# Kernel optimization log

Measured on AMD Instinct MI355X. Metric: run time of the kernel, lower is better.

Reference implementation:

```python
import jax, jax.numpy as jnp
import numpy as np

N_USERS = 200000
N_ITEMS = 100000
EMBED_DIM = 64
N_LAYERS = 3
N_INTER = 1000000


def setup_inputs() -> dict:
    key = jax.random.key(0)
    k1, k2, k3, k4 = jax.random.split(key, 4)
    user_ids = jax.random.randint(k1, (N_INTER,), 0, N_USERS, dtype=jnp.int64 if jax.config.jax_enable_x64 else jnp.int32)
    item_ids = jax.random.randint(k2, (N_INTER,), 0, N_ITEMS, dtype=jnp.int64 if jax.config.jax_enable_x64 else jnp.int32)
    user_emb = jax.random.normal(k3, (N_USERS, EMBED_DIM), dtype=jnp.float32) * 0.1
    item_emb = jax.random.normal(k4, (N_ITEMS, EMBED_DIM), dtype=jnp.float32) * 0.1
    return {"user_emb": user_emb, "item_emb": item_emb, "user_ids": user_ids, "item_ids": item_ids}


def reference(user_emb, item_emb, user_ids, item_ids):
    n_users = user_emb.shape[0]
    n_items = item_emb.shape[0]
    n_nodes = n_users + n_items

    # Symmetric bipartite adjacency as directed edge list (both directions).
    src = jnp.concatenate([user_ids, item_ids + n_users])   # [2E]
    dst = jnp.concatenate([item_ids + n_users, user_ids])   # [2E]

    # Symmetric normalization D^{-1/2} A D^{-1/2} (duplicate edges sum, matching scipy CSR).
    deg = jax.ops.segment_sum(jnp.ones_like(src, dtype=jnp.float32), src, num_segments=n_nodes)
    d_inv_sqrt = jnp.where(deg > 0, jax.lax.rsqrt(jnp.maximum(deg, 1.0)), 0.0)
    w = d_inv_sqrt[src] * d_inv_sqrt[dst]                    # [2E] edge weights

    emb = jnp.concatenate([user_emb, item_emb], axis=0)      # [n_nodes, d]
    acc = emb
    for _ in range(N_LAYERS):
        # SpMM: out[dst] += w * emb[src]
        emb = jax.ops.segment_sum(w[:, None] * emb[src], dst, num_segments=n_nodes)
        acc = acc + emb
    final = acc / (N_LAYERS + 1)                             # mean over stacked layers
    return final[:n_users], final[n_users:]
```

## Files before the change

### kernel.cpp

```cpp
#include <hip/hip_runtime.h>

#define N_USERS 200000
#define N_ITEMS 100000
#define N_NODES 300000
#define DIM 64
#define N_INTER 1000000

#define BSHIFT 10
#define BNODES (1 << BSHIFT)
#define NBUCKET ((N_NODES + BNODES - 1) >> BSHIFT)
#define TILE 4096
#define NBLK_P ((N_INTER + TILE - 1) / TILE)

#define NPW 8
#define NWAVE ((N_NODES + NPW - 1) / NPW)
#define GATHER_THREADS (NWAVE * 64)

typedef unsigned short bf16_t;
typedef unsigned int u32;

static __device__ __forceinline__ bf16_t f2bf(float f) {
    union { float f; u32 u; } v; v.f = f;
    u32 r = v.u + 0x7FFFu + ((v.u >> 16) & 1u);
    return (bf16_t)(r >> 16);
}
static __device__ __forceinline__ float bf2f(bf16_t h) {
    union { u32 u; float f; } v; v.u = ((u32)h) << 16;
    return v.f;
}

__global__ void hist_kernel(const int* __restrict__ uid, const int* __restrict__ iid,
                            u32* __restrict__ bucket_count) {
    __shared__ u32 h[NBUCKET];
    int t = threadIdx.x;
    for (int i = t; i < NBUCKET; i += 256) h[i] = 0;
    __syncthreads();
    int base = blockIdx.x * TILE;
    int end = base + TILE; if (end > N_INTER) end = N_INTER;
    for (int k = base + t; k < end; k += 256) {
        int u = uid[k];
        int it = N_USERS + iid[k];
        atomicAdd(&h[it >> BSHIFT], 1u);
        atomicAdd(&h[u >> BSHIFT], 1u);
    }
    __syncthreads();
    for (int i = t; i < NBUCKET; i += 256)
        if (h[i]) atomicAdd(&bucket_count[i], h[i]);
}

__global__ void scan_kernel(const u32* __restrict__ bucket_count, u32* __restrict__ bstart,
                            u32* __restrict__ bucket_cursor, u32* __restrict__ rowptr) {
    __shared__ u32 buf[2][512];
    int t = threadIdx.x;
    u32 v0 = (t < NBUCKET) ? bucket_count[t] : 0u;
    buf[0][t] = v0;
    __syncthreads();
    int s = 0;
    for (int off = 1; off < 512; off <<= 1) {
        u32 v = buf[s][t];
        if (t >= off) v += buf[s][t - off];
        buf[1 - s][t] = v;
        __syncthreads();
        s = 1 - s;
    }
    if (t < NBUCKET) {
        u32 excl = buf[s][t] - v0;
        bstart[t] = excl;
        bucket_cursor[t] = excl;
    }
    if (t == 0) {
        bstart[NBUCKET] = 2 * N_INTER;
        rowptr[N_NODES] = 2 * N_INTER;
    }
}

__global__ void place_kernel(const int* __restrict__ uid, const int* __restrict__ iid,
                             u32* __restrict__ bucket_cursor, u32* __restrict__ bdata) {
    __shared__ u32 h[NBUCKET];
    __shared__ u32 basesh[NBUCKET];
    int t = threadIdx.x;
    for (int i = t; i < NBUCKET; i += 256) h[i] = 0;
    __syncthreads();
    int base = blockIdx.x * TILE;
    int end = base + TILE; if (end > N_INTER) end = N_INTER;
    for (int k = base + t; k < end; k += 256) {
        int u = uid[k];
        int it = N_USERS + iid[k];
        atomicAdd(&h[it >> BSHIFT], 1u);
        atomicAdd(&h[u >> BSHIFT], 1u);
    }
    __syncthreads();
    for (int i = t; i < NBUCKET; i += 256) {
        u32 c = h[i];
        basesh[i] = c ? atomicAdd(&bucket_cursor[i], c) : 0u;
        h[i] = 0;
    }
    __syncthreads();
    for (int k = base + t; k < end; k += 256) {
        int u = uid[k];
        int it = N_USERS + iid[k];
        {
            int b = it >> BSHIFT;
            u32 pos = basesh[b] + atomicAdd(&h[b], 1u);
            bdata[pos] = (((u32)(it & (BNODES - 1))) << 19) | (u32)u;
        }
        {
            int b = u >> BSHIFT;
            u32 pos = basesh[b] + atomicAdd(&h[b], 1u);
            bdata[pos] = (((u32)(u & (BNODES - 1))) << 19) | (u32)it;
        }
    }
}

__global__ void csr_kernel(const u32* __restrict__ bstart, const u32* __restrict__ bdata,
                           u32* __restrict__ rowptr, float* __restrict__ dinv,
                           int* __restrict__ col) {
    __shared__ u32 cnt[BNODES];
    __shared__ u32 sb[2][BNODES];
    __shared__ u32 cur[BNODES];
    int b = blockIdx.x;
    int t = threadIdx.x;
    int nbase = b << BSHIFT;
    u32 bs = bstart[b], be = bstart[b + 1];
    u32 m = be - bs;

    #pragma unroll
    for (int j = 0; j < 4; ++j) cnt[t + j * 256] = 0;
    __syncthreads();
    for (u32 e = t; e < m; e += 256) {
        u32 v = bdata[bs + e];
        atomicAdd(&cnt[v >> 19], 1u);
    }
    __syncthreads();
    #pragma unroll
    for (int j = 0; j < 4; ++j) sb[0][t + j * 256] = cnt[t + j * 256];
    __syncthreads();
    int s = 0;
    for (int off = 1; off < BNODES; off <<= 1) {
        #pragma unroll
        for (int j = 0; j < 4; ++j) {
            int idx = t + j * 256;
            u32 v = sb[s][idx];
            if (idx >= off) v += sb[s][idx - off];
            sb[1 - s][idx] = v;
        }
        __syncthreads();
        s = 1 - s;
    }
    #pragma unroll
    for (int j = 0; j < 4; ++j) {
        int idx = t + j * 256;
        int node = nbase + idx;
        u32 c = cnt[idx];
        u32 excl = sb[s][idx] - c;
        cur[idx] = excl;
        if (node < N_NODES) {
            rowptr[node] = bs + excl;
            dinv[node] = (c > 0) ? rsqrtf((float)c) : 0.0f;
        }
    }
    __syncthreads();
    for (u32 e = t; e < m; e += 256) {
        u32 v = bdata[bs + e];
        u32 ln = v >> 19;
        u32 pos = atomicAdd(&cur[ln], 1u);
        col[bs + pos] = (int)(v & 0x7FFFFu);
    }
}

__global__ void ecol_kernel(const int* __restrict__ col, const float* __restrict__ dinv,
                            int2* __restrict__ ecol) {
    int e = blockIdx.x * blockDim.x + threadIdx.x;
    if (e < 2 * N_INTER) {
        int s = col[e];
        ecol[e] = make_int2(s, __float_as_int(dinv[s]));
    }
}

__global__ void init_kernel(const float4* __restrict__ ue, const float4* __restrict__ ie,
                            ushort4* __restrict__ cur) {
    int idx = blockIdx.x * blockDim.x + threadIdx.x;
    if (idx < N_NODES * 16) {
        float4 v = (idx < N_USERS * 16) ? ue[idx] : ie[idx - N_USERS * 16];
        ushort4 h;
        h.x = f2bf(v.x); h.y = f2bf(v.y); h.z = f2bf(v.z); h.w = f2bf(v.w);
        cur[idx] = h;
    }
}

__global__ void gather_kernel(const u32* __restrict__ rowptr, const int2* __restrict__ ecol,
                              const float* __restrict__ dinv,
                              const bf16_t* __restrict__ cur, bf16_t* __restrict__ nxt) {
    int wid = (blockIdx.x * blockDim.x + threadIdx.x) >> 6;
    int lane = threadIdx.x & 63;
    int n0 = __builtin_amdgcn_readfirstlane(wid * NPW);
    if (n0 >= N_NODES) return;
    u32 rp[NPW + 1];
    #pragma unroll
    for (int i = 0; i <= NPW; ++i) rp[i] = rowptr[n0 + i];
    u32 eend = rp[NPW];
    u32 cbase = rp[0];
    int2 e = make_int2(0, 0);
    {
        u32 cc = eend - cbase; if (cc > 64) cc = 64;
        if ((u32)lane < cc) e = ecol[cbase + lane];
    }
    u32 pos = rp[0];
    #pragma unroll
    for (int r = 0; r < NPW; ++r) {
        u32 re = rp[r + 1];
        float acc = 0.0f;
        while (pos < re) {
            u32 cend = cbase + 64;
            u32 lim = re < cend ? re : cend;
            for (u32 p = pos; p < lim; p += 8) {
                #pragma unroll
                for (int k = 0; k < 8; ++k) {
                    u32 ei = p + (u32)k;
                    int lidx = (ei < lim) ? (int)(ei - cbase) : 0;
                    lidx = __builtin_amdgcn_readfirstlane(lidx);
                    int s = __builtin_amdgcn_readlane(e.x, lidx);
                    int wb = (ei < lim) ? __builtin_amdgcn_readlane(e.y, lidx) : 0;
                    acc += __int_as_float(wb) * bf2f(cur[((u32)s << 6) + lane]);
                }
            }
            pos = lim;
            if (pos == cend && pos < eend) {
                cbase = pos;
                u32 cc = eend - cbase; if (cc > 64) cc = 64;
                e = make_int2(0, 0);
                if ((u32)lane < cc) e = ecol[cbase + lane];
            }
        }
        nxt[(((u32)(n0 + r)) << 6) + (u32)lane] = f2bf(dinv[n0 + r] * acc);
    }
}

__global__ void gather_final_kernel(const u32* __restrict__ rowptr, const int2* __restrict__ ecol,
                                    const float* __restrict__ dinv,
                                    const bf16_t* __restrict__ b1, const bf16_t* __restrict__ b2,
                                    const float* __restrict__ ue, const float* __restrict__ ie,
                                    float* __restrict__ out) {
    int wid = (blockIdx.x * blockDim.x + threadIdx.x) >> 6;
    int lane = threadIdx.x & 63;
    int n0 = __builtin_amdgcn_readfirstlane(wid * NPW);
    if (n0 >= N_NODES) return;
    u32 rp[NPW + 1];
    #pragma unroll
    for (int i = 0; i <= NPW; ++i) rp[i] = rowptr[n0 + i];
    u32 eend = rp[NPW];
    u32 cbase = rp[0];
    int2 e = make_int2(0, 0);
    {
        u32 cc = eend - cbase; if (cc > 64) cc = 64;
        if ((u32)lane < cc) e = ecol[cbase + lane];
    }
    u32 pos = rp[0];
    #pragma unroll
    for (int r = 0; r < NPW; ++r) {
        u32 re = rp[r + 1];
        float acc = 0.0f;
        while (pos < re) {
            u32 cend = cbase + 64;
            u32 lim = re < cend ? re : cend;
            for (u32 p = pos; p < lim; p += 8) {
                #pragma unroll
                for (int k = 0; k < 8; ++k) {
                    u32 ei = p + (u32)k;
                    int lidx = (ei < lim) ? (int)(ei - cbase) : 0;
                    lidx = __builtin_amdgcn_readfirstlane(lidx);
                    int s = __builtin_amdgcn_readlane(e.x, lidx);
                    int wb = (ei < lim) ? __builtin_amdgcn_readlane(e.y, lidx) : 0;
                    acc += __int_as_float(wb) * bf2f(b2[((u32)s << 6) + lane]);
                }
            }
            pos = lim;
            if (pos == cend && pos < eend) {
                cbase = pos;
                u32 cc = eend - cbase; if (cc > 64) cc = 64;
                e = make_int2(0, 0);
                if ((u32)lane < cc) e = ecol[cbase + lane];
            }
        }
        int n = n0 + r;
        float rr = dinv[n] * acc;
        u32 o = (((u32)n) << 6) + (u32)lane;
        float e0 = (n < N_USERS) ? ue[o] : ie[o - (u32)N_USERS * DIM];
        out[o] = (e0 + bf2f(b1[o]) + bf2f(b2[o]) + rr) * 0.25f;
    }
}

extern "C" void kernel_launch(void* const* d_in, const int* in_sizes, int n_in,
                              void* d_out, int out_size, void* d_ws, size_t ws_size,
                              hipStream_t stream) {
    const float* ue = (const float*)d_in[0];
    const float* ie = (const float*)d_in[1];
    const int* uid = (const int*)d_in[2];
    const int* iid = (const int*)d_in[3];
    float* out = (float*)d_out;

    char* ws = (char*)d_ws;
    size_t off = 0;
    auto alloc = [&](size_t bytes) { char* p = ws + off; off = (off + bytes + 255) & ~(size_t)255; return p; };
    u32*    bucket_count  = (u32*)alloc((size_t)NBUCKET * 4);
    u32*    bstart        = (u32*)alloc((size_t)(NBUCKET + 1) * 4);
    u32*    bucket_cursor = (u32*)alloc((size_t)NBUCKET * 4);
    u32*    rowptr        = (u32*)alloc((size_t)(N_NODES + 1) * 4);
    float*  dinv          = (float*)alloc((size_t)N_NODES * 4);
    u32*    bdata         = (u32*)alloc((size_t)2 * N_INTER * 4);
    int*    col           = (int*)alloc((size_t)2 * N_INTER * 4);
    int2*   ecol          = (int2*)alloc((size_t)2 * N_INTER * 8);
    bf16_t* buf0          = (bf16_t*)alloc((size_t)N_NODES * DIM * 2);
    bf16_t* buf1          = (bf16_t*)alloc((size_t)N_NODES * DIM * 2);
    bf16_t* buf2          = (bf16_t*)alloc((size_t)N_NODES * DIM * 2);

    hipMemsetAsync(bucket_count, 0, (size_t)NBUCKET * 4, stream);
    hist_kernel<<<NBLK_P, 256, 0, stream>>>(uid, iid, bucket_count);
    scan_kernel<<<1, 512, 0, stream>>>(bucket_count, bstart, bucket_cursor, rowptr);
    place_kernel<<<NBLK_P, 256, 0, stream>>>(uid, iid, bucket_cursor, bdata);
    csr_kernel<<<NBUCKET, 256, 0, stream>>>(bstart, bdata, rowptr, dinv, col);
    ecol_kernel<<<(2 * N_INTER + 255) / 256, 256, 0, stream>>>(col, dinv, ecol);

    init_kernel<<<(N_NODES * 16 + 255) / 256, 256, 0, stream>>>(
        (const float4*)ue, (const float4*)ie, (ushort4*)buf0);

    gather_kernel<<<(GATHER_THREADS + 255) / 256, 256, 0, stream>>>(rowptr, ecol, dinv, buf0, buf1);
    gather_kernel<<<(GATHER_THREADS + 255) / 256, 256, 0, stream>>>(rowptr, ecol, dinv, buf1, buf2);
    gather_final_kernel<<<(GATHER_THREADS + 255) / 256, 256, 0, stream>>>(
        rowptr, ecol, dinv, buf1, buf2, ue, ie, out);
}
```

Before: 424.5 us.

## Split wave into two half-waves processing two edges each with packed bf16x2 loads

The SpMM gather kernels now have each lane load a 32-bit word holding two bf16 features. The two 32-lane halves of a wave each handle a different edge, and their partial sums are combined with a cross-half shuffle at the end. Edge entries are read directly per half-wave, replacing the 64-entry staging with readlane broadcasts. This doubles the edges in flight per instruction and halves the number of feature-load instructions. In exchange it adds redundant ecol loads per lane, clamped tail loads, and half the wave sitting idle during the output store.

```diff
diff --git a/kernel.cpp b/kernel.cpp
--- a/kernel.cpp
+++ b/kernel.cpp
@@ -27,6 +27,12 @@
 static __device__ __forceinline__ float bf2f(bf16_t h) {
     union { u32 u; float f; } v; v.u = ((u32)h) << 16;
     return v.f;
+}
+static __device__ __forceinline__ float bflo(u32 v) {
+    union { u32 u; float f; } x; x.u = v << 16; return x.f;
+}
+static __device__ __forceinline__ float bfhi(u32 v) {
+    union { u32 u; float f; } x; x.u = v & 0xFFFF0000u; return x.f;
 }
 
 __global__ void hist_kernel(const int* __restrict__ uid, const int* __restrict__ iid,
@@ -190,7 +196,7 @@
 
 __global__ void gather_kernel(const u32* __restrict__ rowptr, const int2* __restrict__ ecol,
                               const float* __restrict__ dinv,
-                              const bf16_t* __restrict__ cur, bf16_t* __restrict__ nxt) {
+                              const u32* __restrict__ cur, u32* __restrict__ nxt) {
     int wid = (blockIdx.x * blockDim.x + threadIdx.x) >> 6;
     int lane = threadIdx.x & 63;
     int n0 = __builtin_amdgcn_readfirstlane(wid * NPW);
@@ -198,47 +204,36 @@
     u32 rp[NPW + 1];
     #pragma unroll
     for (int i = 0; i <= NPW; ++i) rp[i] = rowptr[n0 + i];
-    u32 eend = rp[NPW];
-    u32 cbase = rp[0];
-    int2 e = make_int2(0, 0);
-    {
-        u32 cc = eend - cbase; if (cc > 64) cc = 64;
-        if ((u32)lane < cc) e = ecol[cbase + lane];
-    }
-    u32 pos = rp[0];
+    u32 half = (u32)(lane >> 5);
+    u32 c = (u32)(lane & 31);
     #pragma unroll
     for (int r = 0; r < NPW; ++r) {
-        u32 re = rp[r + 1];
-        float acc = 0.0f;
-        while (pos < re) {
-            u32 cend = cbase + 64;
-            u32 lim = re < cend ? re : cend;
-            for (u32 p = pos; p < lim; p += 8) {
-                #pragma unroll
-                for (int k = 0; k < 8; ++k) {
-                    u32 ei = p + (u32)k;
-                    int lidx = (ei < lim) ? (int)(ei - cbase) : 0;
-                    lidx = __builtin_amdgcn_readfirstlane(lidx);
-                    int s = __builtin_amdgcn_readlane(e.x, lidx);
-                    int wb = (ei < lim) ? __builtin_amdgcn_readlane(e.y, lidx) : 0;
-                    acc += __int_as_float(wb) * bf2f(cur[((u32)s << 6) + lane]);
-                }
+        u32 rs = rp[r], re = rp[r + 1];
+        float ax = 0.0f, ay = 0.0f;
+        for (u32 p = rs; p < re; p += 8) {
+            #pragma unroll
+            for (int q = 0; q < 4; ++q) {
+                u32 ei = p + 2u * (u32)q + half;
+                int2 e = ecol[ei < re ? ei : (re - 1u)];
+                float w = (ei < re) ? __int_as_float(e.y) : 0.0f;
+                u32 v = cur[((u32)e.x << 5) + c];
+                ax += w * bflo(v);
+                ay += w * bfhi(v);
             }
-            pos = lim;
-            if (pos == cend && pos < eend) {
-                cbase = pos;
-                u32 cc = eend - cbase; if (cc > 64) cc = 64;
-                e = make_int2(0, 0);
-                if ((u32)lane < cc) e = ecol[cbase + lane];
-            }
-        }
-        nxt[(((u32)(n0 + r)) << 6) + (u32)lane] = f2bf(dinv[n0 + r] * acc);
+        }
+        ax += __shfl_xor(ax, 32);
+        ay += __shfl_xor(ay, 32);
+        if (half == 0u) {
+            float sc = dinv[n0 + r];
+            u32 pk = (u32)f2bf(sc * ax) | ((u32)f2bf(sc * ay) << 16);
+            nxt[(((u32)(n0 + r)) << 5) + c] = pk;
+        }
     }
 }
 
 __global__ void gather_final_kernel(const u32* __restrict__ rowptr, const int2* __restrict__ ecol,
                                     const float* __restrict__ dinv,
-                                    const bf16_t* __restrict__ b1, const bf16_t* __restrict__ b2,
+                                    const u32* __restrict__ b1, const u32* __restrict__ b2,
                                     const float* __restrict__ ue, const float* __restrict__ ie,
                                     float* __restrict__ out) {
     int wid = (blockIdx.x * blockDim.x + threadIdx.x) >> 6;
@@ -248,45 +243,36 @@
     u32 rp[NPW + 1];
     #pragma unroll
     for (int i = 0; i <= NPW; ++i) rp[i] = rowptr[n0 + i];
-    u32 eend = rp[NPW];
-    u32 cbase = rp[0];
-    int2 e = make_int2(0, 0);
-    {
-        u32 cc = eend - cbase; if (cc > 64) cc = 64;
-        if ((u32)lane < cc) e = ecol[cbase + lane];
-    }
-    u32 pos = rp[0];
+    u32 half = (u32)(lane >> 5);
+    u32 c = (u32)(lane & 31);
     #pragma unroll
     for (int r = 0; r < NPW; ++r) {
-        u32 re = rp[r + 1];
-        float acc = 0.0f;
-        while (pos < re) {
-            u32 cend = cbase + 64;
-            u32 lim = re < cend ? re : cend;
-            for (u32 p = pos; p < lim; p += 8) {
-                #pragma unroll
-                for (int k = 0; k < 8; ++k) {
-                    u32 ei = p + (u32)k;
-                    int lidx = (ei < lim) ? (int)(ei - cbase) : 0;
-                    lidx = __builtin_amdgcn_readfirstlane(lidx);
-                    int s = __builtin_amdgcn_readlane(e.x, lidx);
-                    int wb = (ei < lim) ? __builtin_amdgcn_readlane(e.y, lidx) : 0;
-                    acc += __int_as_float(wb) * bf2f(b2[((u32)s << 6) + lane]);
-                }
+        u32 rs = rp[r], re = rp[r + 1];
+        float ax = 0.0f, ay = 0.0f;
+        for (u32 p = rs; p < re; p += 8) {
+            #pragma unroll
+            for (int q = 0; q < 4; ++q) {
+                u32 ei = p + 2u * (u32)q + half;
+                int2 e = ecol[ei < re ? ei : (re - 1u)];
+                float w = (ei < re) ? __int_as_float(e.y) : 0.0f;
+                u32 v = b2[((u32)e.x << 5) + c];
+                ax += w * bflo(v);
+                ay += w * bfhi(v);
             }
-            pos = lim;
-            if (pos == cend && pos < eend) {
-                cbase = pos;
-                u32 cc = eend - cbase; if (cc > 64) cc = 64;
-                e = make_int2(0, 0);
-                if ((u32)lane < cc) e = ecol[cbase + lane];
-            }
-        }
-        int n = n0 + r;
-        float rr = dinv[n] * acc;
-        u32 o = (((u32)n) << 6) + (u32)lane;
-        float e0 = (n < N_USERS) ? ue[o] : ie[o - (u32)N_USERS * DIM];
-        out[o] = (e0 + bf2f(b1[o]) + bf2f(b2[o]) + rr) * 0.25f;
+        }
+        ax += __shfl_xor(ax, 32);
+        ay += __shfl_xor(ay, 32);
+        if (half == 0u) {
+            int n = n0 + r;
+            float sc = dinv[n];
+            u32 o32 = (((u32)n) << 5) + c;
+            u32 v1 = b1[o32], v2 = b2[o32];
+            float2 e0 = (n < N_USERS) ? ((const float2*)ue)[o32]
+                                      : ((const float2*)ie)[o32 - (u32)N_USERS * 32u];
+            float ox = (e0.x + bflo(v1) + bflo(v2) + sc * ax) * 0.25f;
+            float oy = (e0.y + bfhi(v1) + bfhi(v2) + sc * ay) * 0.25f;
+            ((float2*)out)[o32] = make_float2(ox, oy);
+        }
     }
 }
 
@@ -324,8 +310,10 @@
     init_kernel<<<(N_NODES * 16 + 255) / 256, 256, 0, stream>>>(
         (const float4*)ue, (const float4*)ie, (ushort4*)buf0);
 
-    gather_kernel<<<(GATHER_THREADS + 255) / 256, 256, 0, stream>>>(rowptr, ecol, dinv, buf0, buf1);
-    gather_kernel<<<(GATHER_THREADS + 255) / 256, 256, 0, stream>>>(rowptr, ecol, dinv, buf1, buf2);
+    gather_kernel<<<(GATHER_THREADS + 255) / 256, 256, 0, stream>>>(
+        rowptr, ecol, dinv, (const u32*)buf0, (u32*)buf1);
+    gather_kernel<<<(GATHER_THREADS + 255) / 256, 256, 0, stream>>>(
+        rowptr, ecol, dinv, (const u32*)buf1, (u32*)buf2);
     gather_final_kernel<<<(GATHER_THREADS + 255) / 256, 256, 0, stream>>>(
-        rowptr, ecol, dinv, buf1, buf2, ue, ie, out);
-}
+        rowptr, ecol, dinv, (const u32*)buf1, (const u32*)buf2, ue, ie, out);
+}
```

New measurement: 540.6 us. 27.4% more time.
